# Kernel optimization log

Hardware: AMD Instinct MI355X
Metric: run time of the kernel (lower is better)

Reference implementation:

```python
import jax, jax.numpy as jnp
import numpy as np

N_NODES = 100000
N_EDGES = 600000
N_GRAPHS = 256
HID = 128
IN_DIM = 7
POCKET_DIM = 28
BN_EPS = 1e-5


def setup_inputs() -> dict:
    key = jax.random.key(0)
    ks = jax.random.split(key, 24)
    d = {}
    d['x'] = jax.random.normal(ks[0], (N_NODES, IN_DIM), dtype=jnp.float32)
    d['edge_index'] = jax.random.randint(ks[1], (2, N_EDGES), 0, N_NODES, dtype=jnp.int32)
    d['batch'] = jnp.sort(jax.random.randint(ks[2], (N_NODES,), 0, N_GRAPHS, dtype=jnp.int32))
    d['pocket'] = jax.random.normal(ks[3], (POCKET_DIM,), dtype=jnp.float32)
    # GCN layer weights (PyG GCNConv: lin then normalized aggregation, bias after)
    def glorot(k, shape):
        lim = np.sqrt(6.0 / (shape[0] + shape[1]))
        return jax.random.uniform(k, shape, jnp.float32, -lim, lim)
    d['W0'] = glorot(ks[4], (IN_DIM, HID)); d['b0'] = jnp.zeros((HID,), jnp.float32)
    d['W1'] = glorot(ks[5], (HID, HID)); d['b1'] = jnp.zeros((HID,), jnp.float32)
    d['W2'] = glorot(ks[6], (HID, HID)); d['b2'] = jnp.zeros((HID,), jnp.float32)
    # BatchNorm (eval mode) params for 3 layers
    d['bn_gamma'] = jax.random.uniform(ks[7], (3, HID), jnp.float32, 0.5, 1.5)
    d['bn_beta'] = 0.1 * jax.random.normal(ks[8], (3, HID), dtype=jnp.float32)
    d['bn_mean'] = 0.1 * jax.random.normal(ks[9], (3, HID), dtype=jnp.float32)
    d['bn_var'] = jax.random.uniform(ks[10], (3, HID), jnp.float32, 0.5, 1.5)
    # pocket MLP: 28 -> 64 -> 64
    d['pw1'] = glorot(ks[11], (POCKET_DIM, 64)); d['pb1'] = jnp.zeros((64,), jnp.float32)
    d['pw2'] = glorot(ks[12], (64, 64)); d['pb2'] = jnp.zeros((64,), jnp.float32)
    # classifier: 192 -> 96 -> 1
    d['cw1'] = glorot(ks[13], (HID + 64, 96)); d['cb1'] = jnp.zeros((96,), jnp.float32)
    d['cw2'] = glorot(ks[14], (96, 1)); d['cb2'] = jnp.zeros((1,), jnp.float32)
    return d


def reference(x, edge_index, batch, pocket, W0, b0, W1, b1, W2, b2,
              bn_gamma, bn_beta, bn_mean, bn_var,
              pw1, pb1, pw2, pb2, cw1, cb1, cw2, cb2):
    src, dst = edge_index[0], edge_index[1]
    n = x.shape[0]
    # degree with self-loops (GCNConv default add_self_loops=True)
    deg = jax.ops.segment_sum(jnp.ones((src.shape[0],), x.dtype), dst, num_segments=n) + 1.0
    dinv = jax.lax.rsqrt(deg)                      # [N]
    norm = dinv[src] * dinv[dst]                   # [E] edge normalization
    self_norm = (dinv * dinv)[:, None]             # [N,1] self-loop norm

    h = x
    for i, (W, b) in enumerate(((W0, b0), (W1, b1), (W2, b2))):
        hl = h @ W                                  # [N,HID]
        agg = jax.ops.segment_sum(hl[src] * norm[:, None], dst, num_segments=n)
        agg = agg + hl * self_norm + b
        # BatchNorm1d in eval mode with running stats
        bn = (agg - bn_mean[i]) * (bn_gamma[i] * jax.lax.rsqrt(bn_var[i] + BN_EPS)) + bn_beta[i]
        h = jax.nn.relu(bn)                         # dropout is identity in eval

    # global mean pool over graphs
    sums = jax.ops.segment_sum(h, batch, num_segments=N_GRAPHS)          # [B,HID]
    cnts = jax.ops.segment_sum(jnp.ones((n,), h.dtype), batch, num_segments=N_GRAPHS)
    lig = sums / jnp.maximum(cnts, 1.0)[:, None]

    # pocket MLP, broadcast to batch
    p = jax.nn.relu(pocket @ pw1 + pb1) @ pw2 + pb2                      # [64]
    pe = jnp.broadcast_to(p[None, :], (N_GRAPHS, 64))

    emb = jnp.concatenate([lig, pe], axis=1)                             # [B,192]
    logits = (jax.nn.relu(emb @ cw1 + cb1) @ cw2 + cb2)[:, 0]            # [B]
    return logits
```

## Files before the change

kernel.cpp:

```cpp
#include <hip/hip_runtime.h>

#define NN 100000
#define NE 600000
#define NG 256
#define HID 128
#define BN_EPS 1e-5f

#define SCAN_TILE 1024
#define NTILES ((NN + SCAN_TILE - 1) / SCAN_TILE)
#define MM_TILES (NN / 32)

typedef __attribute__((ext_vector_type(8))) short short8;
typedef __attribute__((ext_vector_type(4))) float float4v;

__device__ __forceinline__ unsigned short f2bf_rn(float f) {
    unsigned u = __float_as_uint(f);
    unsigned r = u + 0x7FFFu + ((u >> 16) & 1u);
    return (unsigned short)(r >> 16);
}
__device__ __forceinline__ float bf2f(unsigned short h) {
    return __uint_as_float((unsigned)h << 16);
}
__device__ __forceinline__ void unpack8(uint4 u, float* f) {
    f[0] = __uint_as_float(u.x << 16); f[1] = __uint_as_float(u.x & 0xFFFF0000u);
    f[2] = __uint_as_float(u.y << 16); f[3] = __uint_as_float(u.y & 0xFFFF0000u);
    f[4] = __uint_as_float(u.z << 16); f[5] = __uint_as_float(u.z & 0xFFFF0000u);
    f[6] = __uint_as_float(u.w << 16); f[7] = __uint_as_float(u.w & 0xFFFF0000u);
}


__global__ __launch_bounds__(256) void hist_kernel(const int* __restrict__ dst, int* __restrict__ cnt) {
    int e = blockIdx.x * blockDim.x + threadIdx.x;
    if (e < NE) atomicAdd(&cnt[dst[e]], 1);
}


__global__ __launch_bounds__(256) void scan_a(const int* __restrict__ cnt, int* __restrict__ rs,
                                              int* __restrict__ tsum, float* __restrict__ dinv,
                                              int* __restrict__ dbin) {
    __shared__ int s[256];
    __shared__ int hb[64];
    int t = threadIdx.x;
    int base = blockIdx.x * SCAN_TILE;
    int idx = base + t * 4;
    int v0 = (idx + 0 < NN) ? cnt[idx + 0] : 0;
    int v1 = (idx + 1 < NN) ? cnt[idx + 1] : 0;
    int v2 = (idx + 2 < NN) ? cnt[idx + 2] : 0;
    int v3 = (idx + 3 < NN) ? cnt[idx + 3] : 0;
    if (idx + 0 < NN) dinv[idx + 0] = rsqrtf((float)v0 + 1.0f);
    if (idx + 1 < NN) dinv[idx + 1] = rsqrtf((float)v1 + 1.0f);
    if (idx + 2 < NN) dinv[idx + 2] = rsqrtf((float)v2 + 1.0f);
    if (idx + 3 < NN) dinv[idx + 3] = rsqrtf((float)v3 + 1.0f);
    int local = v0 + v1 + v2 + v3;
    s[t] = local;
    if (t < 64) hb[t] = 0;
    __syncthreads();
    if (idx + 0 < NN) atomicAdd(&hb[v0 < 63 ? v0 : 63], 1);
    if (idx + 1 < NN) atomicAdd(&hb[v1 < 63 ? v1 : 63], 1);
    if (idx + 2 < NN) atomicAdd(&hb[v2 < 63 ? v2 : 63], 1);
    if (idx + 3 < NN) atomicAdd(&hb[v3 < 63 ? v3 : 63], 1);
    for (int off = 1; off < 256; off <<= 1) {
        int x = (t >= off) ? s[t - off] : 0;
        __syncthreads();
        s[t] += x;
        __syncthreads();
    }
    int pre = s[t] - local;
    if (t == 255) tsum[blockIdx.x] = s[255];
    if (t < 64 && hb[t]) atomicAdd(&dbin[t], hb[t]);
    if (idx + 0 < NN) rs[idx + 0] = pre; pre += v0;
    if (idx + 1 < NN) rs[idx + 1] = pre; pre += v1;
    if (idx + 2 < NN) rs[idx + 2] = pre; pre += v2;
    if (idx + 3 < NN) rs[idx + 3] = pre;
}


__global__ __launch_bounds__(256) void scan_c(int* __restrict__ rs, const int* __restrict__ tsum,
                                              int* __restrict__ cursor, const int* __restrict__ dbin,
                                              int* __restrict__ dcur, int* __restrict__ perm) {
    __shared__ int s[256];
    __shared__ int pb[64];
    __shared__ int lb[64];
    int t = threadIdx.x;
    s[t] = (t < (int)blockIdx.x && t < NTILES) ? tsum[t] : 0;
    if (t < 64) { lb[t] = 0; pb[t] = dbin[t]; }
    __syncthreads();
#pragma unroll
    for (int off = 128; off >= 1; off >>= 1) {
        if (t < off) s[t] += s[t + off];
        __syncthreads();
    }
    int tile_off = s[0];
    for (int o = 1; o < 64; o <<= 1) {
        int x = (t < 64 && t >= o) ? pb[t - o] : 0;
        __syncthreads();
        if (t < 64) pb[t] += x;
        __syncthreads();
    }
    int base = blockIdx.x * SCAN_TILE;
    int deg[4], rk[4];
#pragma unroll
    for (int k = 0; k < 4; k++) {
        int idx = base + t * 4 + k;
        deg[k] = 0; rk[k] = 0;
        if (idx < NN) {
            int d = cursor[idx];
            deg[k] = (d < 63) ? d : 63;
            rk[k] = atomicAdd(&lb[deg[k]], 1);
        }
    }
    __syncthreads();
    if (t < 64) lb[t] = (pb[t] - dbin[t]) + atomicAdd(&dcur[t], lb[t]);
    __syncthreads();
#pragma unroll
    for (int k = 0; k < 4; k++) {
        int idx = base + t * 4 + k;
        if (idx < NN) {
            int v = rs[idx] + tile_off;
            rs[idx] = v;
            cursor[idx] = v;
            perm[lb[deg[k]] + rk[k]] = idx;
        }
    }
    if (blockIdx.x == 0 && t == 0) rs[NN] = NE;
}


__global__ __launch_bounds__(256) void bucket_prep_kernel(const int* __restrict__ src, const int* __restrict__ dst,
                                                          int* __restrict__ cursor, int* __restrict__ esrc,
                                                          const float* __restrict__ W1, const float* __restrict__ W2,
                                                          unsigned short* __restrict__ w1hi, unsigned short* __restrict__ w1lo,
                                                          unsigned short* __restrict__ w2hi, unsigned short* __restrict__ w2lo,
                                                          const float* __restrict__ pocket,
                                                          const float* __restrict__ pw1, const float* __restrict__ pb1,
                                                          const float* __restrict__ pw2, const float* __restrict__ pb2,
                                                          float* __restrict__ pv, int nb) {
    if ((int)blockIdx.x < nb) {
        int e = blockIdx.x * 256 + threadIdx.x;
        if (e < NE) {
            int pos = atomicAdd(&cursor[dst[e]], 1);
            esrc[pos] = src[e];
        }
    } else if ((int)blockIdx.x < nb + 64) {
        int t = (blockIdx.x - nb) * 256 + threadIdx.x;
        int k = t >> 7, n = t & 127;
        int to = n * HID + k;
        float v1 = W1[t];
        unsigned short h1 = f2bf_rn(v1);
        w1hi[to] = h1;
        w1lo[to] = f2bf_rn(v1 - bf2f(h1));
        float v2 = W2[t];
        unsigned short h2 = f2bf_rn(v2);
        w2hi[to] = h2;
        w2lo[to] = f2bf_rn(v2 - bf2f(h2));
    } else {
        __shared__ float t1[64];
        int j = threadIdx.x;
        if (j < 64) {
            float acc = pb1[j];
            for (int k = 0; k < 28; k++) acc = fmaf(pocket[k], pw1[k * 64 + j], acc);
            t1[j] = fmaxf(acc, 0.f);
        }
        __syncthreads();
        if (j < 64) {
            float acc2 = pb2[j];
            for (int k = 0; k < 64; k++) acc2 = fmaf(t1[k], pw2[k * 64 + j], acc2);
            pv[j] = acc2;
        }
    }
}


template<int N>
__device__ __forceinline__ void bitonic_net(int* a) {
#pragma unroll
    for (int k = 2; k <= N; k <<= 1) {
#pragma unroll
        for (int j = k >> 1; j > 0; j >>= 1) {
#pragma unroll
            for (int i = 0; i < N; i++) {
                int l = i ^ j;
                if (l > i) {
                    int x = a[i], y = a[l];
                    bool up = ((i & k) == 0);
                    bool sw = (x > y) == up;
                    a[i] = sw ? y : x;
                    a[l] = sw ? x : y;
                }
            }
        }
    }
}

template<int N>
__device__ __forceinline__ void sort_reg(int* __restrict__ esrc, int e0, int d) {
    int a[N];
#pragma unroll
    for (int i = 0; i < N; i++) a[i] = (i < d) ? esrc[e0 + i] : 0x7FFFFFFF;
    bitonic_net<N>(a);
#pragma unroll
    for (int i = 0; i < N; i++) if (i < d) esrc[e0 + i] = a[i];
}

__global__ __launch_bounds__(256) void sort_buckets(const int* __restrict__ rs,
                                                    int* __restrict__ esrc,
                                                    const int* __restrict__ perm) {
    int slot = blockIdx.x * 256 + threadIdx.x;
    if (slot >= NN) return;
    int n = perm[slot];
    int e0 = rs[n], e1 = rs[n + 1];
    int d = e1 - e0;
    if (d <= 1) return;
    if (d <= 8) {
        sort_reg<8>(esrc, e0, d);
    } else if (d <= 16) {
        sort_reg<16>(esrc, e0, d);
    } else if (d <= 32) {
        sort_reg<32>(esrc, e0, d);
    } else {
        for (int i = e0 + 1; i < e1; i++) {
            int key = esrc[i];
            int j = i - 1;
            while (j >= e0 && esrc[j] > key) { esrc[j + 1] = esrc[j]; j--; }
            esrc[j + 1] = key;
        }
    }
}


__global__ __launch_bounds__(256) void l0_fused(const float* __restrict__ x,
                                                const int* __restrict__ rs,
                                                const int* __restrict__ esrc,
                                                const float* __restrict__ dinv,
                                                const float* __restrict__ W,
                                                const float* __restrict__ b,
                                                const float* __restrict__ gamma,
                                                const float* __restrict__ beta,
                                                const float* __restrict__ mean,
                                                const float* __restrict__ var,
                                                unsigned short* __restrict__ ohi) {
    int c4 = threadIdx.x & 31;
    int r8 = threadIdx.x >> 5;
    float w[7][4];
#pragma unroll
    for (int k = 0; k < 7; k++)
#pragma unroll
        for (int i = 0; i < 4; i++) w[k][i] = W[k * HID + c4 * 4 + i];
    float4 bb = ((const float4*)b)[c4];
    float4 ga = ((const float4*)gamma)[c4];
    float4 be = ((const float4*)beta)[c4];
    float4 me = ((const float4*)mean)[c4];
    float4 va = ((const float4*)var)[c4];
    float4 sc;
    sc.x = ga.x * rsqrtf(va.x + BN_EPS);
    sc.y = ga.y * rsqrtf(va.y + BN_EPS);
    sc.z = ga.z * rsqrtf(va.z + BN_EPS);
    sc.w = ga.w * rsqrtf(va.w + BN_EPS);
    int m = threadIdx.x >> 3, f = threadIdx.x & 7;
    __shared__ float s[32][8];
    int n0 = blockIdx.x * 32;
    float acc = 0.f;
    int n = n0 + m;
    if (f < 7) {
        float di = dinv[n];
        acc = x[n * 7 + f] * di * di;
        int e0 = rs[n], e1 = rs[n + 1];
        int e = e0;
        for (; e + 1 < e1; e += 2) {
            int s0 = esrc[e], s1 = esrc[e + 1];
            float w0 = dinv[s0] * di, w1 = dinv[s1] * di;
            float a0 = x[s0 * 7 + f];
            float a1 = x[s1 * 7 + f];
            acc = fmaf(a0, w0, acc);
            acc = fmaf(a1, w1, acc);
        }
        if (e < e1) {
            int s0 = esrc[e];
            acc = fmaf(x[s0 * 7 + f], dinv[s0] * di, acc);
        }
    }
    s[m][f] = acc;
    __syncthreads();
#pragma unroll
    for (int g = 0; g < 4; g++) {
        int m2 = g * 8 + r8;
        float o0 = bb.x, o1 = bb.y, o2 = bb.z, o3 = bb.w;
#pragma unroll
        for (int k = 0; k < 7; k++) {
            float xv = s[m2][k];
            o0 = fmaf(xv, w[k][0], o0);
            o1 = fmaf(xv, w[k][1], o1);
            o2 = fmaf(xv, w[k][2], o2);
            o3 = fmaf(xv, w[k][3], o3);
        }
        ushort4 hi4;
        hi4.x = f2bf_rn(fmaxf(fmaf(o0 - me.x, sc.x, be.x), 0.f));
        hi4.y = f2bf_rn(fmaxf(fmaf(o1 - me.y, sc.y, be.y), 0.f));
        hi4.z = f2bf_rn(fmaxf(fmaf(o2 - me.z, sc.z, be.z), 0.f));
        hi4.w = f2bf_rn(fmaxf(fmaf(o3 - me.w, sc.w, be.w), 0.f));
        *(ushort4*)(ohi + (size_t)(n0 + m2) * HID + c4 * 4) = hi4;
    }
}


__global__ __launch_bounds__(256) void mm_mfma(const unsigned short* __restrict__ A,
                                               const unsigned short* __restrict__ Whi,
                                               const unsigned short* __restrict__ Wlo,
                                               unsigned short* __restrict__ out) {
    int wave = threadIdx.x >> 6;
    int lane = threadIdx.x & 63;
    int mrow = lane & 15;
    int quad = lane >> 4;
    int n0 = wave * 32;

    short8 bh[2][4], bl[2][4];
#pragma unroll
    for (int ct = 0; ct < 2; ct++) {
#pragma unroll
        for (int kc = 0; kc < 4; kc++) {
            size_t off = (size_t)(n0 + ct * 16 + mrow) * HID + kc * 32 + quad * 8;
            bh[ct][kc] = *(const short8*)(Whi + off);
            bl[ct][kc] = *(const short8*)(Wlo + off);
        }
    }

    int tile = blockIdx.x;
    if (tile >= MM_TILES) return;

    short8 ah[2][4];
#pragma unroll
    for (int rt = 0; rt < 2; rt++)
#pragma unroll
        for (int kc = 0; kc < 4; kc++)
            ah[rt][kc] = *(const short8*)(A + (size_t)(tile * 32 + rt * 16 + mrow) * HID + kc * 32 + quad * 8);

    for (;;) {
        int nt = tile + gridDim.x;
        bool has_next = nt < MM_TILES;
        short8 an[2][4];
        if (has_next) {
#pragma unroll
            for (int rt = 0; rt < 2; rt++)
#pragma unroll
                for (int kc = 0; kc < 4; kc++)
                    an[rt][kc] = *(const short8*)(A + (size_t)(nt * 32 + rt * 16 + mrow) * HID + kc * 32 + quad * 8);
        }

        float4v acc[2][2];
#pragma unroll
        for (int rt = 0; rt < 2; rt++)
#pragma unroll
            for (int ct = 0; ct < 2; ct++) {
                acc[rt][ct].x = 0.f; acc[rt][ct].y = 0.f;
                acc[rt][ct].z = 0.f; acc[rt][ct].w = 0.f;
            }

#pragma unroll
        for (int kc = 0; kc < 4; kc++)
#pragma unroll
            for (int rt = 0; rt < 2; rt++)
#pragma unroll
                for (int ct = 0; ct < 2; ct++) {
                    acc[rt][ct] = __builtin_amdgcn_mfma_f32_16x16x32_bf16(ah[rt][kc], bh[ct][kc], acc[rt][ct], 0, 0, 0);
                    acc[rt][ct] = __builtin_amdgcn_mfma_f32_16x16x32_bf16(ah[rt][kc], bl[ct][kc], acc[rt][ct], 0, 0, 0);
                }

        int m0 = tile * 32;
#pragma unroll
        for (int rt = 0; rt < 2; rt++)
#pragma unroll
            for (int ct = 0; ct < 2; ct++) {
                int col = n0 + ct * 16 + mrow;
#pragma unroll
                for (int r = 0; r < 4; r++) {
                    int row = m0 + rt * 16 + quad * 4 + r;
                    out[(size_t)row * HID + col] = f2bf_rn(acc[rt][ct][r]);
                }
            }

        if (!has_next) break;
#pragma unroll
        for (int rt = 0; rt < 2; rt++)
#pragma unroll
            for (int kc = 0; kc < 4; kc++) ah[rt][kc] = an[rt][kc];
        tile = nt;
    }
}


__global__ __launch_bounds__(256) void gather_bn(const unsigned short* __restrict__ hl,
                                                 const int* __restrict__ rs,
                                                 const int* __restrict__ esrc,
                                                 const float* __restrict__ dinv,
                                                 const float* __restrict__ b,
                                                 const float* __restrict__ gamma,
                                                 const float* __restrict__ beta,
                                                 const float* __restrict__ mean,
                                                 const float* __restrict__ var,
                                                 unsigned short* __restrict__ ohi) {
    int t = blockIdx.x * blockDim.x + threadIdx.x;
    int lane = t & 15;
    int n = t >> 4;
    if (n >= NN) return;
    const uint4* hlv = (const uint4*)hl;
    float di = dinv[n];
    float dsq = di * di;

    float acc[8], v[8];
    {
        uint4 sv = hlv[(size_t)n * 16 + lane];
        unpack8(sv, v);
        float4 bA = ((const float4*)b)[lane * 2];
        float4 bB = ((const float4*)b)[lane * 2 + 1];
        acc[0] = fmaf(v[0], dsq, bA.x); acc[1] = fmaf(v[1], dsq, bA.y);
        acc[2] = fmaf(v[2], dsq, bA.z); acc[3] = fmaf(v[3], dsq, bA.w);
        acc[4] = fmaf(v[4], dsq, bB.x); acc[5] = fmaf(v[5], dsq, bB.y);
        acc[6] = fmaf(v[6], dsq, bB.z); acc[7] = fmaf(v[7], dsq, bB.w);
    }

    int e0 = rs[n], e1 = rs[n + 1];
    int e = e0;
    for (; e + 3 < e1; e += 4) {
        int s0 = esrc[e], s1 = esrc[e + 1], s2 = esrc[e + 2], s3 = esrc[e + 3];
        float w0 = dinv[s0] * di, w1 = dinv[s1] * di;
        float w2 = dinv[s2] * di, w3 = dinv[s3] * di;
        uint4 u0 = hlv[(size_t)s0 * 16 + lane];
        uint4 u1 = hlv[(size_t)s1 * 16 + lane];
        uint4 u2 = hlv[(size_t)s2 * 16 + lane];
        uint4 u3 = hlv[(size_t)s3 * 16 + lane];
        unpack8(u0, v);
#pragma unroll
        for (int i = 0; i < 8; i++) acc[i] = fmaf(v[i], w0, acc[i]);
        unpack8(u1, v);
#pragma unroll
        for (int i = 0; i < 8; i++) acc[i] = fmaf(v[i], w1, acc[i]);
        unpack8(u2, v);
#pragma unroll
        for (int i = 0; i < 8; i++) acc[i] = fmaf(v[i], w2, acc[i]);
        unpack8(u3, v);
#pragma unroll
        for (int i = 0; i < 8; i++) acc[i] = fmaf(v[i], w3, acc[i]);
    }
    for (; e < e1; e++) {
        int s0 = esrc[e];
        float w0 = dinv[s0] * di;
        uint4 u0 = hlv[(size_t)s0 * 16 + lane];
        unpack8(u0, v);
#pragma unroll
        for (int i = 0; i < 8; i++) acc[i] = fmaf(v[i], w0, acc[i]);
    }

    float4 gA = ((const float4*)gamma)[lane * 2], gB = ((const float4*)gamma)[lane * 2 + 1];
    float4 eA = ((const float4*)beta)[lane * 2],  eB = ((const float4*)beta)[lane * 2 + 1];
    float4 mA = ((const float4*)mean)[lane * 2],  mB = ((const float4*)mean)[lane * 2 + 1];
    float4 vA = ((const float4*)var)[lane * 2],   vB = ((const float4*)var)[lane * 2 + 1];
    float o[8];
    o[0] = fmaxf(fmaf(acc[0] - mA.x, gA.x * rsqrtf(vA.x + BN_EPS), eA.x), 0.f);
    o[1] = fmaxf(fmaf(acc[1] - mA.y, gA.y * rsqrtf(vA.y + BN_EPS), eA.y), 0.f);
    o[2] = fmaxf(fmaf(acc[2] - mA.z, gA.z * rsqrtf(vA.z + BN_EPS), eA.z), 0.f);
    o[3] = fmaxf(fmaf(acc[3] - mA.w, gA.w * rsqrtf(vA.w + BN_EPS), eA.w), 0.f);
    o[4] = fmaxf(fmaf(acc[4] - mB.x, gB.x * rsqrtf(vB.x + BN_EPS), eB.x), 0.f);
    o[5] = fmaxf(fmaf(acc[5] - mB.y, gB.y * rsqrtf(vB.y + BN_EPS), eB.y), 0.f);
    o[6] = fmaxf(fmaf(acc[6] - mB.z, gB.z * rsqrtf(vB.z + BN_EPS), eB.z), 0.f);
    o[7] = fmaxf(fmaf(acc[7] - mB.w, gB.w * rsqrtf(vB.w + BN_EPS), eB.w), 0.f);

    uint4 p;
    p.x = (unsigned)f2bf_rn(o[0]) | ((unsigned)f2bf_rn(o[1]) << 16);
    p.y = (unsigned)f2bf_rn(o[2]) | ((unsigned)f2bf_rn(o[3]) << 16);
    p.z = (unsigned)f2bf_rn(o[4]) | ((unsigned)f2bf_rn(o[5]) << 16);
    p.w = (unsigned)f2bf_rn(o[6]) | ((unsigned)f2bf_rn(o[7]) << 16);
    ((uint4*)ohi)[(size_t)n * 16 + lane] = p;
}


__global__ __launch_bounds__(1024) void poolcls_kernel(const unsigned short* __restrict__ h,
                                                       const int* __restrict__ batch,
                                                       const float* __restrict__ pv,
                                                       const float* __restrict__ cw1,
                                                       const float* __restrict__ cb1,
                                                       const float* __restrict__ cw2,
                                                       const float* __restrict__ cb2,
                                                       float* __restrict__ out) {
    int g = blockIdx.x;
    int lane = threadIdx.x & 31;
    int row = threadIdx.x >> 5;
    __shared__ int se[2];
    __shared__ float emb[192];
    __shared__ float hid[96];
    if (threadIdx.x < 2) {
        int target = g + threadIdx.x;
        int lo = 0, hi = NN;
        while (lo < hi) {
            int mid = (lo + hi) >> 1;
            if (batch[mid] < target) lo = mid + 1; else hi = mid;
        }
        se[threadIdx.x] = lo;
    }
    if (threadIdx.x < 64) emb[128 + threadIdx.x] = pv[threadIdx.x];
    __syncthreads();
    int start = se[0], end = se[1];
    const uint2* h2 = (const uint2*)h;
    float4 acc = make_float4(0.f, 0.f, 0.f, 0.f);
    for (int n = start + row; n < end; n += 32) {
        uint2 u = h2[(size_t)n * 32 + lane];
        acc.x += __uint_as_float(u.x << 16);
        acc.y += __uint_as_float(u.x & 0xFFFF0000u);
        acc.z += __uint_as_float(u.y << 16);
        acc.w += __uint_as_float(u.y & 0xFFFF0000u);
    }
    __shared__ float4 part[32][32];
    part[row][lane] = acc;
    __syncthreads();
#pragma unroll
    for (int off = 16; off >= 1; off >>= 1) {
        if (row < off) {
            float4 a = part[row][lane];
            float4 c = part[row + off][lane];
            a.x += c.x; a.y += c.y; a.z += c.z; a.w += c.w;
            part[row][lane] = a;
        }
        __syncthreads();
    }
    if (row == 0) {
        float inv = 1.0f / fmaxf((float)(end - start), 1.0f);
        float4 a = part[0][lane];
        a.x *= inv; a.y *= inv; a.z *= inv; a.w *= inv;
        ((float4*)emb)[lane] = a;
    }
    __syncthreads();
    int j = threadIdx.x;
    if (j < 96) {
        float a = cb1[j];
        for (int k = 0; k < 192; k++) a = fmaf(emb[k], cw1[k * 96 + j], a);
        hid[j] = fmaxf(a, 0.f) * cw2[j];
    }
    __syncthreads();
    if (j == 0) {
        float s = cb2[0];
        for (int k = 0; k < 96; k++) s += hid[k];
        out[g] = s;
    }
}

extern "C" void kernel_launch(void* const* d_in, const int* in_sizes, int n_in,
                              void* d_out, int out_size, void* d_ws, size_t ws_size,
                              hipStream_t stream) {
    const float* x        = (const float*)d_in[0];
    const int*   eidx     = (const int*)d_in[1];
    const int*   batch    = (const int*)d_in[2];
    const float* pocket   = (const float*)d_in[3];
    const float* W0 = (const float*)d_in[4];
    const float* b0 = (const float*)d_in[5];
    const float* W1 = (const float*)d_in[6];
    const float* b1 = (const float*)d_in[7];
    const float* W2 = (const float*)d_in[8];
    const float* b2 = (const float*)d_in[9];
    const float* bn_gamma = (const float*)d_in[10];
    const float* bn_beta  = (const float*)d_in[11];
    const float* bn_mean  = (const float*)d_in[12];
    const float* bn_var   = (const float*)d_in[13];
    const float* pw1 = (const float*)d_in[14]; const float* pb1 = (const float*)d_in[15];
    const float* pw2 = (const float*)d_in[16]; const float* pb2 = (const float*)d_in[17];
    const float* cw1 = (const float*)d_in[18]; const float* cb1 = (const float*)d_in[19];
    const float* cw2 = (const float*)d_in[20]; const float* cb2 = (const float*)d_in[21];
    float* out = (float*)d_out;

    float* ws   = (float*)d_ws;
    float* dinv = ws;
    int*   cnt  = (int*)(ws + NN);
    int*   rs   = cnt + NN;
    int*   tsum = rs + NN + 1;
    int*   dbin = tsum + 128;
    int*   dcur = dbin + 64;
    int*   perm = dcur + 64;
    int*   esrc = perm + NN;
    unsigned short* w1hi = (unsigned short*)(esrc + NE);
    unsigned short* w1lo = w1hi + HID * HID;
    unsigned short* w2hi = w1lo + HID * HID;
    unsigned short* w2lo = w2hi + HID * HID;
    size_t head = (size_t)NN * 2 + (NN + 1) + 128 + 64 + 64 + NN + NE + (4 * HID * HID) / 2;
    head = (head + 3) & ~(size_t)3;
    unsigned short* A = (unsigned short*)(ws + head);
    unsigned short* B = A + (size_t)NN * HID;
    float* pv   = (float*)(B + (size_t)NN * HID);

    const int* srcp = eidx;
    const int* dstp = eidx + NE;

    const int NB = (NE + 255) / 256;

    hipMemsetAsync(cnt, 0, (size_t)(NN + NN + 1 + 128 + 64 + 64) * sizeof(int), stream);
    hist_kernel<<<NB, 256, 0, stream>>>(dstp, cnt);
    scan_a<<<NTILES, 256, 0, stream>>>(cnt, rs, tsum, dinv, dbin);
    scan_c<<<NTILES, 256, 0, stream>>>(rs, tsum, cnt, dbin, dcur, perm);
    bucket_prep_kernel<<<NB + 65, 256, 0, stream>>>(srcp, dstp, cnt, esrc,
                                                    W1, W2, w1hi, w1lo, w2hi, w2lo,
                                                    pocket, pw1, pb1, pw2, pb2, pv, NB);
    sort_buckets<<<(NN + 255) / 256, 256, 0, stream>>>(rs, esrc, perm);

    l0_fused<<<MM_TILES, 256, 0, stream>>>(x, rs, esrc, dinv, W0, b0,
                                           bn_gamma + 0 * HID, bn_beta + 0 * HID,
                                           bn_mean + 0 * HID, bn_var + 0 * HID, A);

    const int MM_BLOCKS = 1024;
    const int GA_BLOCKS = (NN * 16 + 255) / 256;

    mm_mfma<<<MM_BLOCKS, 256, 0, stream>>>(A, w1hi, w1lo, B);
    gather_bn<<<GA_BLOCKS, 256, 0, stream>>>(
        B, rs, esrc, dinv, b1,
        bn_gamma + 1 * HID, bn_beta + 1 * HID, bn_mean + 1 * HID, bn_var + 1 * HID, A);
    mm_mfma<<<MM_BLOCKS, 256, 0, stream>>>(A, w2hi, w2lo, B);
    gather_bn<<<GA_BLOCKS, 256, 0, stream>>>(
        B, rs, esrc, dinv, b2,
        bn_gamma + 2 * HID, bn_beta + 2 * HID, bn_mean + 2 * HID, bn_var + 2 * HID, A);

    poolcls_kernel<<<NG, 1024, 0, stream>>>(A, batch, pv, cw1, cb1, cw2, cb2, out);
}
```

Measured before the change: 345.8 us.

## Fuse layer-0 and gather+BN with following MFMA matmul via LDS tiles

Folds the layer-1 matmul into the layer-0 aggregation kernel, and the layer-2 matmul into the layer-1 gather+BN kernel. The intermediate 32-row bf16 tile is staged in shared memory instead of being written to and reread from global memory. This removes two kernel launches and two full N×128 round trips through global memory. In exchange, each block reloads the W hi/lo fragments per tile rather than keeping them across a persistent loop. The gather phase now runs with the fixed block shape the matmul needs, which may reduce latency hiding for the irregular gathers.

```diff
diff --git a/kernel.cpp b/kernel.cpp
--- a/kernel.cpp
+++ b/kernel.cpp
@@ -228,17 +228,21 @@
 }
 
 
-__global__ __launch_bounds__(256) void l0_fused(const float* __restrict__ x,
-                                                const int* __restrict__ rs,
-                                                const int* __restrict__ esrc,
-                                                const float* __restrict__ dinv,
-                                                const float* __restrict__ W,
-                                                const float* __restrict__ b,
-                                                const float* __restrict__ gamma,
-                                                const float* __restrict__ beta,
-                                                const float* __restrict__ mean,
-                                                const float* __restrict__ var,
-                                                unsigned short* __restrict__ ohi) {
+__global__ __launch_bounds__(256) void l0mm1_fused(const float* __restrict__ x,
+                                                   const int* __restrict__ rs,
+                                                   const int* __restrict__ esrc,
+                                                   const float* __restrict__ dinv,
+                                                   const float* __restrict__ W,
+                                                   const float* __restrict__ b,
+                                                   const float* __restrict__ gamma,
+                                                   const float* __restrict__ beta,
+                                                   const float* __restrict__ mean,
+                                                   const float* __restrict__ var,
+                                                   const unsigned short* __restrict__ Whi,
+                                                   const unsigned short* __restrict__ Wlo,
+                                                   unsigned short* __restrict__ out) {
+    __shared__ float s[32][8];
+    __shared__ unsigned short ht[32][136];
     int c4 = threadIdx.x & 31;
     int r8 = threadIdx.x >> 5;
     float w[7][4];
@@ -257,10 +261,9 @@
     sc.z = ga.z * rsqrtf(va.z + BN_EPS);
     sc.w = ga.w * rsqrtf(va.w + BN_EPS);
     int m = threadIdx.x >> 3, f = threadIdx.x & 7;
-    __shared__ float s[32][8];
-    int n0 = blockIdx.x * 32;
+    int n0b = blockIdx.x * 32;
     float acc = 0.f;
-    int n = n0 + m;
+    int n = n0b + m;
     if (f < 7) {
         float di = dinv[n];
         acc = x[n * 7 + f] * di * di;
@@ -298,93 +301,193 @@
         hi4.y = f2bf_rn(fmaxf(fmaf(o1 - me.y, sc.y, be.y), 0.f));
         hi4.z = f2bf_rn(fmaxf(fmaf(o2 - me.z, sc.z, be.z), 0.f));
         hi4.w = f2bf_rn(fmaxf(fmaf(o3 - me.w, sc.w, be.w), 0.f));
-        *(ushort4*)(ohi + (size_t)(n0 + m2) * HID + c4 * 4) = hi4;
-    }
-}
-
-
-__global__ __launch_bounds__(256) void mm_mfma(const unsigned short* __restrict__ A,
-                                               const unsigned short* __restrict__ Whi,
-                                               const unsigned short* __restrict__ Wlo,
-                                               unsigned short* __restrict__ out) {
+        *(ushort4*)&ht[m2][c4 * 4] = hi4;
+    }
+    __syncthreads();
     int wave = threadIdx.x >> 6;
     int lane = threadIdx.x & 63;
     int mrow = lane & 15;
     int quad = lane >> 4;
-    int n0 = wave * 32;
-
+    int cn0 = wave * 32;
     short8 bh[2][4], bl[2][4];
 #pragma unroll
-    for (int ct = 0; ct < 2; ct++) {
+    for (int ct = 0; ct < 2; ct++)
 #pragma unroll
         for (int kc = 0; kc < 4; kc++) {
-            size_t off = (size_t)(n0 + ct * 16 + mrow) * HID + kc * 32 + quad * 8;
+            size_t off = (size_t)(cn0 + ct * 16 + mrow) * HID + kc * 32 + quad * 8;
             bh[ct][kc] = *(const short8*)(Whi + off);
             bl[ct][kc] = *(const short8*)(Wlo + off);
         }
-    }
-
-    int tile = blockIdx.x;
-    if (tile >= MM_TILES) return;
-
     short8 ah[2][4];
 #pragma unroll
     for (int rt = 0; rt < 2; rt++)
 #pragma unroll
         for (int kc = 0; kc < 4; kc++)
-            ah[rt][kc] = *(const short8*)(A + (size_t)(tile * 32 + rt * 16 + mrow) * HID + kc * 32 + quad * 8);
-
-    for (;;) {
-        int nt = tile + gridDim.x;
-        bool has_next = nt < MM_TILES;
-        short8 an[2][4];
-        if (has_next) {
-#pragma unroll
-            for (int rt = 0; rt < 2; rt++)
-#pragma unroll
-                for (int kc = 0; kc < 4; kc++)
-                    an[rt][kc] = *(const short8*)(A + (size_t)(nt * 32 + rt * 16 + mrow) * HID + kc * 32 + quad * 8);
-        }
-
-        float4v acc[2][2];
+            ah[rt][kc] = *(const short8*)&ht[rt * 16 + mrow][kc * 32 + quad * 8];
+    float4v accm[2][2];
+#pragma unroll
+    for (int rt = 0; rt < 2; rt++)
+#pragma unroll
+        for (int ct = 0; ct < 2; ct++) {
+            accm[rt][ct].x = 0.f; accm[rt][ct].y = 0.f;
+            accm[rt][ct].z = 0.f; accm[rt][ct].w = 0.f;
+        }
+#pragma unroll
+    for (int kc = 0; kc < 4; kc++)
 #pragma unroll
         for (int rt = 0; rt < 2; rt++)
 #pragma unroll
             for (int ct = 0; ct < 2; ct++) {
-                acc[rt][ct].x = 0.f; acc[rt][ct].y = 0.f;
-                acc[rt][ct].z = 0.f; acc[rt][ct].w = 0.f;
+                accm[rt][ct] = __builtin_amdgcn_mfma_f32_16x16x32_bf16(ah[rt][kc], bh[ct][kc], accm[rt][ct], 0, 0, 0);
+                accm[rt][ct] = __builtin_amdgcn_mfma_f32_16x16x32_bf16(ah[rt][kc], bl[ct][kc], accm[rt][ct], 0, 0, 0);
             }
-
+#pragma unroll
+    for (int rt = 0; rt < 2; rt++)
+#pragma unroll
+        for (int ct = 0; ct < 2; ct++) {
+            int col = cn0 + ct * 16 + mrow;
+#pragma unroll
+            for (int r = 0; r < 4; r++) {
+                int row = n0b + rt * 16 + quad * 4 + r;
+                out[(size_t)row * HID + col] = f2bf_rn(accm[rt][ct][r]);
+            }
+        }
+}
+
+
+__global__ __launch_bounds__(256) void gmm_fused(const unsigned short* __restrict__ hl,
+                                                 const int* __restrict__ rs,
+                                                 const int* __restrict__ esrc,
+                                                 const float* __restrict__ dinv,
+                                                 const float* __restrict__ b,
+                                                 const float* __restrict__ gamma,
+                                                 const float* __restrict__ beta,
+                                                 const float* __restrict__ mean,
+                                                 const float* __restrict__ var,
+                                                 const unsigned short* __restrict__ Whi,
+                                                 const unsigned short* __restrict__ Wlo,
+                                                 unsigned short* __restrict__ out) {
+    __shared__ unsigned short ht[32][136];
+    int lane16 = threadIdx.x & 15;
+    int nl = threadIdx.x >> 4;
+    int tl = blockIdx.x * 32;
+    const uint4* hlv = (const uint4*)hl;
+    float4 bA = ((const float4*)b)[lane16 * 2],     bB = ((const float4*)b)[lane16 * 2 + 1];
+    float4 gA = ((const float4*)gamma)[lane16 * 2], gB = ((const float4*)gamma)[lane16 * 2 + 1];
+    float4 eA = ((const float4*)beta)[lane16 * 2],  eB = ((const float4*)beta)[lane16 * 2 + 1];
+    float4 mA = ((const float4*)mean)[lane16 * 2],  mB = ((const float4*)mean)[lane16 * 2 + 1];
+    float4 vA = ((const float4*)var)[lane16 * 2],   vB = ((const float4*)var)[lane16 * 2 + 1];
+#pragma unroll
+    for (int pass = 0; pass < 2; pass++) {
+        int nloc = pass * 16 + nl;
+        int n = tl + nloc;
+        float di = dinv[n];
+        float dsq = di * di;
+        float acc[8], v[8];
+        {
+            uint4 sv = hlv[(size_t)n * 16 + lane16];
+            unpack8(sv, v);
+            acc[0] = fmaf(v[0], dsq, bA.x); acc[1] = fmaf(v[1], dsq, bA.y);
+            acc[2] = fmaf(v[2], dsq, bA.z); acc[3] = fmaf(v[3], dsq, bA.w);
+            acc[4] = fmaf(v[4], dsq, bB.x); acc[5] = fmaf(v[5], dsq, bB.y);
+            acc[6] = fmaf(v[6], dsq, bB.z); acc[7] = fmaf(v[7], dsq, bB.w);
+        }
+        int e0 = rs[n], e1 = rs[n + 1];
+        int e = e0;
+        for (; e + 3 < e1; e += 4) {
+            int s0 = esrc[e], s1 = esrc[e + 1], s2 = esrc[e + 2], s3 = esrc[e + 3];
+            float w0 = dinv[s0] * di, w1 = dinv[s1] * di;
+            float w2 = dinv[s2] * di, w3 = dinv[s3] * di;
+            uint4 u0 = hlv[(size_t)s0 * 16 + lane16];
+            uint4 u1 = hlv[(size_t)s1 * 16 + lane16];
+            uint4 u2 = hlv[(size_t)s2 * 16 + lane16];
+            uint4 u3 = hlv[(size_t)s3 * 16 + lane16];
+            unpack8(u0, v);
+#pragma unroll
+            for (int i = 0; i < 8; i++) acc[i] = fmaf(v[i], w0, acc[i]);
+            unpack8(u1, v);
+#pragma unroll
+            for (int i = 0; i < 8; i++) acc[i] = fmaf(v[i], w1, acc[i]);
+            unpack8(u2, v);
+#pragma unroll
+            for (int i = 0; i < 8; i++) acc[i] = fmaf(v[i], w2, acc[i]);
+            unpack8(u3, v);
+#pragma unroll
+            for (int i = 0; i < 8; i++) acc[i] = fmaf(v[i], w3, acc[i]);
+        }
+        for (; e < e1; e++) {
+            int s0 = esrc[e];
+            float w0 = dinv[s0] * di;
+            uint4 u0 = hlv[(size_t)s0 * 16 + lane16];
+            unpack8(u0, v);
+#pragma unroll
+            for (int i = 0; i < 8; i++) acc[i] = fmaf(v[i], w0, acc[i]);
+        }
+        float o[8];
+        o[0] = fmaxf(fmaf(acc[0] - mA.x, gA.x * rsqrtf(vA.x + BN_EPS), eA.x), 0.f);
+        o[1] = fmaxf(fmaf(acc[1] - mA.y, gA.y * rsqrtf(vA.y + BN_EPS), eA.y), 0.f);
+        o[2] = fmaxf(fmaf(acc[2] - mA.z, gA.z * rsqrtf(vA.z + BN_EPS), eA.z), 0.f);
+        o[3] = fmaxf(fmaf(acc[3] - mA.w, gA.w * rsqrtf(vA.w + BN_EPS), eA.w), 0.f);
+        o[4] = fmaxf(fmaf(acc[4] - mB.x, gB.x * rsqrtf(vB.x + BN_EPS), eB.x), 0.f);
+        o[5] = fmaxf(fmaf(acc[5] - mB.y, gB.y * rsqrtf(vB.y + BN_EPS), eB.y), 0.f);
+        o[6] = fmaxf(fmaf(acc[6] - mB.z, gB.z * rsqrtf(vB.z + BN_EPS), eB.z), 0.f);
+        o[7] = fmaxf(fmaf(acc[7] - mB.w, gB.w * rsqrtf(vB.w + BN_EPS), eB.w), 0.f);
+        uint4 p;
+        p.x = (unsigned)f2bf_rn(o[0]) | ((unsigned)f2bf_rn(o[1]) << 16);
+        p.y = (unsigned)f2bf_rn(o[2]) | ((unsigned)f2bf_rn(o[3]) << 16);
+        p.z = (unsigned)f2bf_rn(o[4]) | ((unsigned)f2bf_rn(o[5]) << 16);
+        p.w = (unsigned)f2bf_rn(o[6]) | ((unsigned)f2bf_rn(o[7]) << 16);
+        *(uint4*)&ht[nloc][lane16 * 8] = p;
+    }
+    __syncthreads();
+    int wave = threadIdx.x >> 6;
+    int lane = threadIdx.x & 63;
+    int mrow = lane & 15;
+    int quad = lane >> 4;
+    int cn0 = wave * 32;
+    short8 bh[2][4], bl[2][4];
+#pragma unroll
+    for (int ct = 0; ct < 2; ct++)
+#pragma unroll
+        for (int kc = 0; kc < 4; kc++) {
+            size_t off = (size_t)(cn0 + ct * 16 + mrow) * HID + kc * 32 + quad * 8;
+            bh[ct][kc] = *(const short8*)(Whi + off);
+            bl[ct][kc] = *(const short8*)(Wlo + off);
+        }
+    short8 ah[2][4];
+#pragma unroll
+    for (int rt = 0; rt < 2; rt++)
 #pragma unroll
         for (int kc = 0; kc < 4; kc++)
-#pragma unroll
-            for (int rt = 0; rt < 2; rt++)
-#pragma unroll
-                for (int ct = 0; ct < 2; ct++) {
-                    acc[rt][ct] = __builtin_amdgcn_mfma_f32_16x16x32_bf16(ah[rt][kc], bh[ct][kc], acc[rt][ct], 0, 0, 0);
-                    acc[rt][ct] = __builtin_amdgcn_mfma_f32_16x16x32_bf16(ah[rt][kc], bl[ct][kc], acc[rt][ct], 0, 0, 0);
-                }
-
-        int m0 = tile * 32;
+            ah[rt][kc] = *(const short8*)&ht[rt * 16 + mrow][kc * 32 + quad * 8];
+    float4v accm[2][2];
+#pragma unroll
+    for (int rt = 0; rt < 2; rt++)
+#pragma unroll
+        for (int ct = 0; ct < 2; ct++) {
+            accm[rt][ct].x = 0.f; accm[rt][ct].y = 0.f;
+            accm[rt][ct].z = 0.f; accm[rt][ct].w = 0.f;
+        }
+#pragma unroll
+    for (int kc = 0; kc < 4; kc++)
 #pragma unroll
         for (int rt = 0; rt < 2; rt++)
 #pragma unroll
             for (int ct = 0; ct < 2; ct++) {
-                int col = n0 + ct * 16 + mrow;
-#pragma unroll
-                for (int r = 0; r < 4; r++) {
-                    int row = m0 + rt * 16 + quad * 4 + r;
-                    out[(size_t)row * HID + col] = f2bf_rn(acc[rt][ct][r]);
-                }
+                accm[rt][ct] = __builtin_amdgcn_mfma_f32_16x16x32_bf16(ah[rt][kc], bh[ct][kc], accm[rt][ct], 0, 0, 0);
+                accm[rt][ct] = __builtin_amdgcn_mfma_f32_16x16x32_bf16(ah[rt][kc], bl[ct][kc], accm[rt][ct], 0, 0, 0);
             }
-
-        if (!has_next) break;
-#pragma unroll
-        for (int rt = 0; rt < 2; rt++)
-#pragma unroll
-            for (int kc = 0; kc < 4; kc++) ah[rt][kc] = an[rt][kc];
-        tile = nt;
-    }
+#pragma unroll
+    for (int rt = 0; rt < 2; rt++)
+#pragma unroll
+        for (int ct = 0; ct < 2; ct++) {
+            int col = cn0 + ct * 16 + mrow;
+#pragma unroll
+            for (int r = 0; r < 4; r++) {
+                int row = tl + rt * 16 + quad * 4 + r;
+                out[(size_t)row * HID + col] = f2bf_rn(accm[rt][ct][r]);
+            }
+        }
 }
 
 
@@ -598,21 +701,18 @@
                                                     pocket, pw1, pb1, pw2, pb2, pv, NB);
     sort_buckets<<<(NN + 255) / 256, 256, 0, stream>>>(rs, esrc, perm);
 
-    l0_fused<<<MM_TILES, 256, 0, stream>>>(x, rs, esrc, dinv, W0, b0,
-                                           bn_gamma + 0 * HID, bn_beta + 0 * HID,
-                                           bn_mean + 0 * HID, bn_var + 0 * HID, A);
-
-    const int MM_BLOCKS = 1024;
+    l0mm1_fused<<<MM_TILES, 256, 0, stream>>>(x, rs, esrc, dinv, W0, b0,
+                                              bn_gamma + 0 * HID, bn_beta + 0 * HID,
+                                              bn_mean + 0 * HID, bn_var + 0 * HID,
+                                              w1hi, w1lo, B);
+    gmm_fused<<<MM_TILES, 256, 0, stream>>>(B, rs, esrc, dinv, b1,
+                                            bn_gamma + 1 * HID, bn_beta + 1 * HID,
+                                            bn_mean + 1 * HID, bn_var + 1 * HID,
+                                            w2hi, w2lo, A);
     const int GA_BLOCKS = (NN * 16 + 255) / 256;
-
-    mm_mfma<<<MM_BLOCKS, 256, 0, stream>>>(A, w1hi, w1lo, B);
     gather_bn<<<GA_BLOCKS, 256, 0, stream>>>(
-        B, rs, esrc, dinv, b1,
-        bn_gamma + 1 * HID, bn_beta + 1 * HID, bn_mean + 1 * HID, bn_var + 1 * HID, A);
-    mm_mfma<<<MM_BLOCKS, 256, 0, stream>>>(A, w2hi, w2lo, B);
-    gather_bn<<<GA_BLOCKS, 256, 0, stream>>>(
-        B, rs, esrc, dinv, b2,
-        bn_gamma + 2 * HID, bn_beta + 2 * HID, bn_mean + 2 * HID, bn_var + 2 * HID, A);
-
-    poolcls_kernel<<<NG, 1024, 0, stream>>>(A, batch, pv, cw1, cb1, cw2, cb2, out);
-}
+        A, rs, esrc, dinv, b2,
+        bn_gamma + 2 * HID, bn_beta + 2 * HID, bn_mean + 2 * HID, bn_var + 2 * HID, B);
+
+    poolcls_kernel<<<NG, 1024, 0, stream>>>(B, batch, pv, cw1, cb1, cw2, cb2, out);
+}
```

After: 348.0 us. No clear change (+0.6%).
